# Performance work log

Measured on AMD Instinct MI355X. Metric: run time of the kernel, lower is better.

## Reference

```python
import jax, jax.numpy as jnp
import numpy as np
jax.config.update("jax_enable_x64", True)

PRIMES = [2654435761, 2246822519, 3266489917, 2028178513, 1220703125, 1610612741, 805306457, 402653189, 3674653429, 2860486313, 1073676287, 2971215073, 1500450271, 3267000013, 2654435789, 4049292737]
WINDOWS = [1, 2, 4, 8]
BUCKETS = 2000000
SIGN_BITS = 8
BOUNDARY = 2
OFFSETS = (1, 2, 3, 4, 5, 6, 7, 8)
CHUNK = 32


def layer_norm(x, w, b, eps=1e-5):
    m = jnp.mean(x, axis=-1, keepdims=True)
    v = jnp.var(x, axis=-1, keepdims=True)
    return (x - m) * jax.lax.rsqrt(v + eps) * w + b


def shift_right(tokens, off):
    T = tokens.shape[1]
    return jnp.pad(tokens, ((0, 0), (off, 0)))[:, :T]


def hash_scale(tokens, window):
    # rolling polynomial hash: XOR of prime-multiplied shifted tokens
    h = jnp.zeros_like(tokens)
    for i in range(window):
        off = i + 1
        if off >= tokens.shape[1]:
            continue
        h = h ^ (shift_right(tokens, off) * PRIMES[i % len(PRIMES)])
    return h % BUCKETS


def tiny_scan(x, gw, gb, iw, ib, ow, ob, lnw, lnb):
    # chunked cumsum-based linear recurrence h_t = a_t * h_{t-1} + (1-a_t) * u_t
    B, T, D = x.shape
    S = gw.shape[0]
    K = min(CHUNK, T)
    g = jax.nn.sigmoid(jnp.einsum('btd,sd->bts', x, gw) + gb)
    drive = (1.0 - g) * (jnp.einsum('btd,sd->bts', x, iw) + ib)
    nC = T // K  # T chosen divisible by CHUNK
    a = g.reshape(B, nC, K, S)
    b = drive.reshape(B, nC, K, S)
    log_a = jnp.log(jnp.maximum(a, 1e-6))
    cum_a = jnp.exp(jnp.cumsum(log_a, axis=2))             # [B,nC,K,S]
    inv_cum_a = 1.0 / jnp.maximum(cum_a, 1e-8)
    cum_wb = jnp.cumsum(b * inv_cum_a, axis=2)

    def step(h, cs):
        ca, cw = cs                                        # [B,K,S]
        out = ca * (h[:, None, :] + cw)
        return out[:, -1], out

    h0 = jnp.zeros((B, S), x.dtype)
    _, outs = jax.lax.scan(step, h0, (jnp.swapaxes(cum_a, 0, 1), jnp.swapaxes(cum_wb, 0, 1)))
    states = jnp.swapaxes(outs, 0, 1).reshape(B, T, S)
    y = jnp.einsum('bts,ds->btd', states, ow) + ob
    return layer_norm(x + y, lnw, lnb)


def forward(chars, byte_embed, table0, table1, table2, table3, cond_w, conv_w, conv_b,
            gate_w, gate_b, inpr_w, inpr_b, outpr_w, outpr_b, scan_ln_w, scan_ln_b,
            inp_w, inp_b, r_w1, r_w2, r_proj, r_ln_w, r_ln_b, out_w, out_b):
    tokens = chars.astype(jnp.int64)
    B, T = tokens.shape
    tables = [table0, table1, table2, table3]
    keys = [hash_scale(tokens, WINDOWS[s]) for s in range(4)]
    short = [tables[s][keys[s]] for s in range(BOUNDARY)]     # each [B,T,2]
    # condition long-scale keys on sign bits of short-scale features
    cond_logits = jnp.einsum('btd,sd->bts', jnp.concatenate(short, axis=-1), cond_w)
    bits = (cond_logits > 0).astype(jnp.int64)                # [B,T,8]
    cond_key = jnp.zeros((B, T), dtype=jnp.int64)
    for i in range(SIGN_BITS):
        cond_key = cond_key ^ (bits[..., i] * PRIMES[i])
    longe = [tables[s][(keys[s] ^ cond_key) % BUCKETS] for s in range(BOUNDARY, 4)]
    hash_feat = jnp.concatenate(short + longe, axis=-1)       # [B,T,8]
    # causal depthwise conv over hash features
    C = hash_feat.shape[-1]
    ht = jnp.swapaxes(hash_feat, 1, 2)                        # [B,C,T]
    Kc = conv_w.shape[-1]
    conv = jax.lax.conv_general_dilated(ht, conv_w, (1,), [(Kc - 1, 0)],
                                        dimension_numbers=('NCH', 'OIH', 'NCH'),
                                        feature_group_count=C)
    hash_feat = jax.nn.silu(jnp.swapaxes(conv + conv_b[None, :, None], 1, 2))
    byte_emb = byte_embed[tokens]                             # [B,T,64]
    # match features: equality with k-shifted sequence
    mfs = []
    for k in OFFSETS:
        m = (tokens == shift_right(tokens, k)).astype(jnp.float32)
        m = m.at[:, :k].set(0.0)
        mfs.append(m)
    mf = jnp.stack(mfs, axis=-1)                              # [B,T,8]
    h = jnp.concatenate([byte_emb, hash_feat, mf], axis=-1)   # [B,T,80]
    h = tiny_scan(h, gate_w, gate_b, inpr_w, inpr_b, outpr_w, outpr_b, scan_ln_w, scan_ln_b)
    h = jax.nn.silu(jnp.einsum('btd,hd->bth', h, inp_w) + inp_b)   # [B,T,256]
    hh = jnp.einsum('bth,dh->btd',
                    jax.nn.silu(jnp.einsum('btd,hd->bth', h, r_w1)) * jnp.einsum('btd,hd->bth', h, r_w2),
                    r_proj)
    h = layer_norm(hh + h, r_ln_w, r_ln_b)
    return jnp.einsum('bth,vh->btv', h, out_w) + out_b        # [B,T,1024]


def setup_inputs() -> dict:
    key = jax.random.key(0)
    ks = jax.random.split(key, 32)
    f32 = jnp.float32
    B, T, V, EB, S, D, H = 32, 2048, 1024, 64, 32, 80, 256

    def rn(k, shape, std):
        return jax.random.normal(k, shape, dtype=f32) * std

    return {
        'chars': jax.random.randint(ks[0], (B, T), 0, V, dtype=jnp.int64),
        'byte_embed': rn(ks[1], (V, EB), 0.02),
        'table0': rn(ks[2], (BUCKETS, 2), 0.02),
        'table1': rn(ks[3], (BUCKETS, 2), 0.02),
        'table2': rn(ks[4], (BUCKETS, 2), 0.02),
        'table3': rn(ks[5], (BUCKETS, 2), 0.02),
        'cond_w': rn(ks[6], (SIGN_BITS, 2 * BOUNDARY), 0.3),
        'conv_w': rn(ks[7], (8, 1, 8), 0.2),
        'conv_b': rn(ks[8], (8,), 0.02),
        'gate_w': rn(ks[9], (S, D), 0.1),
        'gate_b': rn(ks[10], (S,), 0.02),
        'inpr_w': rn(ks[11], (S, D), 0.1),
        'inpr_b': rn(ks[12], (S,), 0.02),
        'outpr_w': rn(ks[13], (D, S), 0.1),
        'outpr_b': rn(ks[14], (D,), 0.02),
        'scan_ln_w': jnp.ones((D,), f32),
        'scan_ln_b': jnp.zeros((D,), f32),
        'inp_w': rn(ks[15], (H, D), 0.1),
        'inp_b': rn(ks[16], (H,), 0.02),
        'r_w1': rn(ks[17], (H, H), 0.05),
        'r_w2': rn(ks[18], (H, H), 0.05),
        'r_proj': rn(ks[19], (H, H), 0.05),
        'r_ln_w': jnp.ones((H,), f32),
        'r_ln_b': jnp.zeros((H,), f32),
        'out_w': rn(ks[20], (V, H), 0.05),
        'out_b': rn(ks[21], (V,), 0.02),
    }


def reference(chars, byte_embed, table0, table1, table2, table3, cond_w, conv_w, conv_b,
              gate_w, gate_b, inpr_w, inpr_b, outpr_w, outpr_b, scan_ln_w, scan_ln_b,
              inp_w, inp_b, r_w1, r_w2, r_proj, r_ln_w, r_ln_b, out_w, out_b):
    return forward(chars, byte_embed, table0, table1, table2, table3, cond_w, conv_w, conv_b,
                   gate_w, gate_b, inpr_w, inpr_b, outpr_w, outpr_b, scan_ln_w, scan_ln_b,
                   inp_w, inp_b, r_w1, r_w2, r_proj, r_ln_w, r_ln_b, out_w, out_b)
```

## Files before the change

### kernel.cpp

```cpp
#include <hip/hip_runtime.h>

#define BB 32
#define TT 2048
#define SS 32
#define DD 80
#define HH 256
#define VV 1024
#define EBD 64

typedef unsigned short u16;
typedef __attribute__((ext_vector_type(8))) __bf16 bf16x8;
typedef __attribute__((ext_vector_type(4))) float f32x4;

#define MFMA(a, b, c) __builtin_amdgcn_mfma_f32_16x16x32_bf16(a, b, c, 0, 0, 0)

__device__ inline u16 f2bu(float f) {
    unsigned u = __float_as_uint(f);
    return (u16)((u + 0x7FFFu + ((u >> 16) & 1u)) >> 16);
}
__device__ inline __bf16 f2b(float f) {
    u16 r = f2bu(f);
    return __builtin_bit_cast(__bf16, r);
}
__device__ inline float b2f(u16 h) { return __uint_as_float(((unsigned)h) << 16); }

__device__ inline bf16x8 ldfrag(const u16* base, int row, int k0, int lane) {
    return *(const bf16x8*)(base + (size_t)row * 256 + k0 + ((lane >> 4) << 3));
}
__device__ inline bf16x8 ldfrag96(const u16* base, int row, int k0, int lane) {
    return *(const bf16x8*)(base + (size_t)row * 96 + k0 + ((lane >> 4) << 3));
}

__global__ __launch_bounds__(256) void k_prep(const float* __restrict__ w1,
                                              const float* __restrict__ w2,
                                              const float* __restrict__ wp,
                                              const float* __restrict__ ow,
                                              const float* __restrict__ iw,
                                              u16* __restrict__ wbf) {
    int i = blockIdx.x * 256 + threadIdx.x;
    if (i >= 483328) return;
    float v;
    if (i < 65536) v = w1[i];
    else if (i < 131072) v = w2[i - 65536];
    else if (i < 196608) v = wp[i - 131072];
    else if (i < 458752) v = ow[i - 196608];
    else {
        int j = i - 458752;
        int row = j / 96, col = j % 96;
        v = (col < 80) ? iw[row * 80 + col] : 0.f;
    }
    wbf[i] = f2bu(v);
}

__global__ __launch_bounds__(256) void k_hash(const int* __restrict__ tok,
                                              const float* __restrict__ t0,
                                              const float* __restrict__ t1,
                                              const float* __restrict__ t2,
                                              const float* __restrict__ t3,
                                              const float* __restrict__ cond_w,
                                              float* __restrict__ raw) {
    int idx = blockIdx.x * 256 + threadIdx.x;
    if (idx >= BB * TT) return;
    int b = idx / TT, t = idx % TT;
    const int* tr = tok + b * TT;

    unsigned long long tv[8];
#pragma unroll
    for (int i = 0; i < 8; i++) {
        int ts = t - 1 - i;
        tv[i] = (ts >= 0) ? (unsigned long long)(unsigned)tr[ts] : 0ull;
    }
    const unsigned long long P[8] = {2654435761ull, 2246822519ull, 3266489917ull,
                                     2028178513ull, 1220703125ull, 1610612741ull,
                                     805306457ull, 402653189ull};
    unsigned long long x = 0ull;
    x ^= tv[0] * P[0]; unsigned long long k0 = x % 2000000ull;
    x ^= tv[1] * P[1]; unsigned long long k1 = x % 2000000ull;
    x ^= tv[2] * P[2]; x ^= tv[3] * P[3]; unsigned long long k2 = x % 2000000ull;
    x ^= tv[4] * P[4]; x ^= tv[5] * P[5];
    x ^= tv[6] * P[6]; x ^= tv[7] * P[7]; unsigned long long k3 = x % 2000000ull;

    float f0 = t0[k0 * 2], f1 = t0[k0 * 2 + 1];
    float f2 = t1[k1 * 2], f3 = t1[k1 * 2 + 1];

    unsigned long long ck = 0ull;
#pragma unroll
    for (int j = 0; j < 8; j++) {
        float lg = f0 * cond_w[j * 4 + 0] + f1 * cond_w[j * 4 + 1] +
                   f2 * cond_w[j * 4 + 2] + f3 * cond_w[j * 4 + 3];
        if (lg > 0.f) ck ^= P[j];
    }
    unsigned long long lk2 = (k2 ^ ck) % 2000000ull;
    unsigned long long lk3 = (k3 ^ ck) % 2000000ull;

    float* o = raw + (size_t)idx * 8;
    o[0] = f0; o[1] = f1; o[2] = f2; o[3] = f3;
    o[4] = t2[lk2 * 2]; o[5] = t2[lk2 * 2 + 1];
    o[6] = t3[lk3 * 2]; o[7] = t3[lk3 * 2 + 1];
}

__global__ __launch_bounds__(256) void k_feat(const int* __restrict__ tok,
                                              const float* __restrict__ be,
                                              const float* __restrict__ raw,
                                              const float* __restrict__ conv_w,
                                              const float* __restrict__ conv_b,
                                              float* __restrict__ hf) {
    int idx = blockIdx.x * 256 + threadIdx.x;
    if (idx >= BB * TT) return;
    int b = idx / TT, t = idx % TT;
    const int* tr = tok + b * TT;
    float* o = hf + (size_t)idx * DD;

    int tk = tr[t];
    const float* ber = be + (size_t)tk * EBD;
#pragma unroll
    for (int q = 0; q < 16; q++) *(f32x4*)(o + q * 4) = *(const f32x4*)(ber + q * 4);

#pragma unroll
    for (int c = 0; c < 8; c++) {
        float acc = conv_b[c];
#pragma unroll
        for (int k = 0; k < 8; k++) {
            int ts = t - 7 + k;
            if (ts >= 0) acc += conv_w[c * 8 + k] * raw[((size_t)(b * TT + ts)) * 8 + c];
        }
        o[64 + c] = acc / (1.f + expf(-acc));
    }

#pragma unroll
    for (int k = 1; k <= 8; k++) {
        float m = (t >= k && tk == tr[t - k]) ? 1.f : 0.f;
        o[71 + k] = m;
    }
}

__global__ __launch_bounds__(256) void k_gates(const float* __restrict__ hf,
                                               const float* __restrict__ gw,
                                               const float* __restrict__ gb,
                                               const float* __restrict__ iw,
                                               const float* __restrict__ ib,
                                               float* __restrict__ Ag,
                                               float* __restrict__ Dr) {
    __shared__ float xs[64][DD];
    __shared__ float gws[32 * 81];
    __shared__ float iws[32 * 81];
    int blk = blockIdx.x;
    int b = blk >> 5;
    int t0 = (blk & 31) << 6;
    const float* src = hf + ((size_t)(b * TT + t0)) * DD;
    for (int i = threadIdx.x; i < 64 * DD; i += 256) xs[i / DD][i % DD] = src[i];
    for (int i = threadIdx.x; i < 32 * 80; i += 256) {
        int s = i / 80, d = i % 80;
        gws[s * 81 + d] = gw[i];
        iws[s * 81 + d] = iw[i];
    }
    __syncthreads();

    for (int p = threadIdx.x; p < 64 * SS; p += 256) {
        int s = p & 31, tt = p >> 5;
        float ga = gb[s], ia = ib[s];
        for (int d = 0; d < DD; d++) {
            float xv = xs[tt][d];
            ga += xv * gws[s * 81 + d];
            ia += xv * iws[s * 81 + d];
        }
        float g = 1.f / (1.f + expf(-ga));
        float drv = (1.f - g) * ia;
        size_t oo = ((size_t)(b * SS + s)) * TT + t0 + tt;
        Ag[oo] = g;
        Dr[oo] = drv;
    }
}

__global__ __launch_bounds__(64) void k_scan_par(const float* __restrict__ Ag,
                                                 const float* __restrict__ Dr,
                                                 float* __restrict__ st) {
    int bs = blockIdx.x;
    int b = bs >> 5, s = bs & 31;
    int c = threadIdx.x;
    const float* ar = Ag + (size_t)bs * TT + c * 32;
    const float* dr = Dr + (size_t)bs * TT + c * 32;

    float ca[32], cw[32];
    float lacc = 0.f, wacc = 0.f;
#pragma unroll
    for (int k = 0; k < 32; k += 4) {
        f32x4 av = *(const f32x4*)(ar + k);
        f32x4 dv = *(const f32x4*)(dr + k);
#pragma unroll
        for (int j = 0; j < 4; j++) {
            lacc += logf(fmaxf(av[j], 1e-6f));
            float cav = expf(lacc);
            ca[k + j] = cav;
            wacc += dv[j] / fmaxf(cav, 1e-8f);
            cw[k + j] = wacc;
        }
    }

    float A = ca[31];
    float Bc = ca[31] * wacc;
    for (int off = 1; off < 64; off <<= 1) {
        float Ap = __shfl_up(A, off, 64);
        float Bp = __shfl_up(Bc, off, 64);
        if (c >= off) {
            Bc = A * Bp + Bc;
            A = A * Ap;
        }
    }
    float h0 = __shfl_up(Bc, 1, 64);
    if (c == 0) h0 = 0.f;

    float* op = st + ((size_t)(b * TT + c * 32)) * SS + s;
#pragma unroll
    for (int k = 0; k < 32; k++)
        op[(size_t)k * SS] = ca[k] * (h0 + cw[k]);
}

__global__ __launch_bounds__(256) void k_post(const float* __restrict__ st,
                                              const float* __restrict__ hf,
                                              const float* __restrict__ ow,
                                              const float* __restrict__ ob,
                                              const float* __restrict__ lnw,
                                              const float* __restrict__ lnb,
                                              u16* __restrict__ h1p) {
    __shared__ float ows[DD * SS];
    for (int i = threadIdx.x; i < DD * SS; i += 256) ows[i] = ow[i];
    __syncthreads();

    int idx = blockIdx.x * 256 + threadIdx.x;
    if (idx >= BB * TT) return;
    const float* sp = st + (size_t)idx * SS;
    float sv[SS];
#pragma unroll
    for (int i = 0; i < SS; i += 4) {
        f32x4 v4 = *(const f32x4*)(sp + i);
        sv[i] = v4[0]; sv[i + 1] = v4[1]; sv[i + 2] = v4[2]; sv[i + 3] = v4[3];
    }
    const float* x = hf + (size_t)idx * DD;

    float s1 = 0.f, s2 = 0.f;
    for (int d = 0; d < DD; d++) {
        float acc = ob[d];
#pragma unroll
        for (int i = 0; i < SS; i++) acc += sv[i] * ows[d * SS + i];
        float v = acc + x[d];
        s1 += v; s2 += v * v;
    }
    float m = s1 * (1.f / DD);
    float var = s2 * (1.f / DD) - m * m;
    float rs = rsqrtf(var + 1e-5f);
    u16* o = h1p + (size_t)idx * 96;
    for (int d = 0; d < DD; d++) {
        float acc = ob[d];
#pragma unroll
        for (int i = 0; i < SS; i++) acc += sv[i] * ows[d * SS + i];
        float v = acc + x[d];
        o[d] = f2bu((v - m) * rs * lnw[d] + lnb[d]);
    }
    *(f32x4*)(o + 80) = f32x4{0.f, 0.f, 0.f, 0.f};
    *(f32x4*)(o + 88) = f32x4{0.f, 0.f, 0.f, 0.f};
}

#define SX 264
__global__ __launch_bounds__(256) void k_gmlp_f(const u16* __restrict__ h1p,
                                                const u16* __restrict__ iwb,
                                                const float* __restrict__ ibias,
                                                const u16* __restrict__ w1,
                                                const u16* __restrict__ w2,
                                                const u16* __restrict__ wp,
                                                const float* __restrict__ lnw,
                                                const float* __restrict__ lnb,
                                                u16* __restrict__ h3) {
    __shared__ u16 Xs[64 * SX];
    __shared__ u16 Us[64 * SX];
    __shared__ float redS[64][4], redQ[64][4];
    int lane = threadIdx.x & 63, wv = threadIdx.x >> 6;
    int r0 = blockIdx.x * 64;
    int g = lane >> 4, cl = lane & 15, rl = lane & 15;

    {
        int c0 = wv * 64;
        f32x4 acc[4][4] = {};
#pragma unroll
        for (int ks = 0; ks < 3; ks++) {
            int k0 = ks * 32;
            bf16x8 a[4];
#pragma unroll
            for (int mi = 0; mi < 4; mi++) a[mi] = ldfrag96(h1p, r0 + mi * 16 + rl, k0, lane);
#pragma unroll
            for (int ni = 0; ni < 4; ni++) {
                bf16x8 b = ldfrag96(iwb, c0 + ni * 16 + rl, k0, lane);
#pragma unroll
                for (int mi = 0; mi < 4; mi++) acc[mi][ni] = MFMA(a[mi], b, acc[mi][ni]);
            }
        }
#pragma unroll
        for (int ni = 0; ni < 4; ni++) {
            float bv = ibias[c0 + ni * 16 + cl];
#pragma unroll
            for (int mi = 0; mi < 4; mi++)
#pragma unroll
                for (int r = 0; r < 4; r++) {
                    float v = acc[mi][ni][r] + bv;
                    Xs[(mi * 16 + g * 4 + r) * SX + c0 + ni * 16 + cl] =
                        f2bu(v / (1.f + expf(-v)));
                }
        }
    }
    __syncthreads();

    for (int cg = 0; cg < 2; cg++) {
        int c0 = cg * 128 + wv * 32;
        f32x4 a1[4][2] = {}, a2[4][2] = {};
        for (int ks = 0; ks < 8; ks++) {
            int k0 = ks * 32 + (g << 3);
            bf16x8 a[4];
#pragma unroll
            for (int mi = 0; mi < 4; mi++)
                a[mi] = *(const bf16x8*)&Xs[(mi * 16 + rl) * SX + k0];
#pragma unroll
            for (int ni = 0; ni < 2; ni++) {
                bf16x8 b1 = ldfrag(w1, c0 + ni * 16 + rl, ks * 32, lane);
                bf16x8 b2 = ldfrag(w2, c0 + ni * 16 + rl, ks * 32, lane);
#pragma unroll
                for (int mi = 0; mi < 4; mi++) {
                    a1[mi][ni] = MFMA(a[mi], b1, a1[mi][ni]);
                    a2[mi][ni] = MFMA(a[mi], b2, a2[mi][ni]);
                }
            }
        }
#pragma unroll
        for (int mi = 0; mi < 4; mi++)
#pragma unroll
            for (int ni = 0; ni < 2; ni++)
#pragma unroll
                for (int r = 0; r < 4; r++) {
                    float v1 = a1[mi][ni][r], v2 = a2[mi][ni][r];
                    float u = v1 / (1.f + expf(-v1)) * v2;
                    Us[(mi * 16 + g * 4 + r) * SX + c0 + ni * 16 + cl] = f2bu(u);
                }
    }
    __syncthreads();

    {
        int c0 = wv * 64;
        f32x4 acc[4][4] = {};
        for (int ks = 0; ks < 8; ks++) {
            int k0 = ks * 32 + (g << 3);
            bf16x8 a[4];
#pragma unroll
            for (int mi = 0; mi < 4; mi++)
                a[mi] = *(const bf16x8*)&Us[(mi * 16 + rl) * SX + k0];
#pragma unroll
            for (int ni = 0; ni < 4; ni++) {
                bf16x8 b = ldfrag(wp, c0 + ni * 16 + rl, ks * 32, lane);
#pragma unroll
                for (int mi = 0; mi < 4; mi++) acc[mi][ni] = MFMA(a[mi], b, acc[mi][ni]);
            }
        }
#pragma unroll
        for (int mi = 0; mi < 4; mi++)
#pragma unroll
            for (int r = 0; r < 4; r++) {
                float s = 0.f, q = 0.f;
                int row = mi * 16 + g * 4 + r;
#pragma unroll
                for (int ni = 0; ni < 4; ni++) {
                    int col = c0 + ni * 16 + cl;
                    float v = acc[mi][ni][r] + b2f(Xs[row * SX + col]);
                    acc[mi][ni][r] = v;
                    s += v; q += v * v;
                }
                for (int m = 1; m < 16; m <<= 1) {
                    s += __shfl_xor(s, m, 64);
                    q += __shfl_xor(q, m, 64);
                }
                if (cl == 0) { redS[row][wv] = s; redQ[row][wv] = q; }
            }
        __syncthreads();

        float lw[4], lb[4];
#pragma unroll
        for (int ni = 0; ni < 4; ni++) {
            lw[ni] = lnw[c0 + ni * 16 + cl];
            lb[ni] = lnb[c0 + ni * 16 + cl];
        }
#pragma unroll
        for (int mi = 0; mi < 4; mi++)
#pragma unroll
            for (int r = 0; r < 4; r++) {
                int row = mi * 16 + g * 4 + r;
                float S = redS[row][0] + redS[row][1] + redS[row][2] + redS[row][3];
                float Q = redQ[row][0] + redQ[row][1] + redQ[row][2] + redQ[row][3];
                float m = S * (1.f / 256.f);
                float rs = rsqrtf(Q * (1.f / 256.f) - m * m + 1e-5f);
#pragma unroll
                for (int ni = 0; ni < 4; ni++) {
                    float y = (acc[mi][ni][r] - m) * rs * lw[ni] + lb[ni];
                    h3[(size_t)(r0 + row) * 256 + c0 + ni * 16 + cl] = f2bu(y);
                }
            }
    }
}

#define SA 40
__global__ __launch_bounds__(256) void k_out4(const u16* __restrict__ h3,
                                              const u16* __restrict__ ow,
                                              const float* __restrict__ bias,
                                              float* __restrict__ out) {
    __shared__ u16 As[2][128 * SA];
    __shared__ u16 Bs[2][128 * SA];
    int tid = threadIdx.x, lane = tid & 63, wv = tid >> 6;
    int r0 = blockIdx.x * 128;
    int wr = (wv >> 1) * 64, wc = (wv & 1) * 64;
    int rl = lane & 15, g = lane >> 4;

    int row0_ = tid >> 2, cc0_ = tid & 3;
    int row1_ = (tid + 256) >> 2, cc1_ = tid & 3;
    bf16x8 rA0, rA1, rB0, rB1;

#define LOADT(cg, kt)                                                                      \
    {                                                                                      \
        int kbase = (kt) * 32;                                                             \
        int c0g = (cg) * 128;                                                              \
        rA0 = *(const bf16x8*)(h3 + (size_t)(r0 + row0_) * 256 + kbase + cc0_ * 8);        \
        rA1 = *(const bf16x8*)(h3 + (size_t)(r0 + row1_) * 256 + kbase + cc1_ * 8);        \
        rB0 = *(const bf16x8*)(ow + (size_t)(c0g + row0_) * 256 + kbase + cc0_ * 8);       \
        rB1 = *(const bf16x8*)(ow + (size_t)(c0g + row1_) * 256 + kbase + cc1_ * 8);       \
    }
#define WRITET(buf)                                                                        \
    {                                                                                      \
        *(bf16x8*)&As[buf][row0_ * SA + cc0_ * 8] = rA0;                                   \
        *(bf16x8*)&As[buf][row1_ * SA + cc1_ * 8] = rA1;                                   \
        *(bf16x8*)&Bs[buf][row0_ * SA + cc0_ * 8] = rB0;                                   \
        *(bf16x8*)&Bs[buf][row1_ * SA + cc1_ * 8] = rB1;                                   \
    }

    for (int cg = 0; cg < 8; cg++) {
        LOADT(cg, 0);
        WRITET(0);
        f32x4 acc[4][4] = {};
        for (int kt = 0; kt < 8; kt++) {
            int buf = kt & 1;
            if (kt < 7) LOADT(cg, kt + 1);
            __syncthreads();
            bf16x8 a[4], b[4];
#pragma unroll
            for (int mi = 0; mi < 4; mi++)
                a[mi] = *(const bf16x8*)&As[buf][(wr + mi * 16 + rl) * SA + g * 8];
#pragma unroll
            for (int ni = 0; ni < 4; ni++)
                b[ni] = *(const bf16x8*)&Bs[buf][(wc + ni * 16 + rl) * SA + g * 8];
#pragma unroll
            for (int ni = 0; ni < 4; ni++)
#pragma unroll
                for (int mi = 0; mi < 4; mi++) acc[mi][ni] = MFMA(a[mi], b[ni], acc[mi][ni]);
            if (kt < 7) WRITET(buf ^ 1);
        }
        int c0g = cg * 128;
        int cl = lane & 15;
#pragma unroll
        for (int ni = 0; ni < 4; ni++) {
            float bv = bias[c0g + wc + ni * 16 + cl];
#pragma unroll
            for (int mi = 0; mi < 4; mi++)
#pragma unroll
                for (int r = 0; r < 4; r++)
                    out[(size_t)(r0 + wr + mi * 16 + g * 4 + r) * VV + c0g + wc + ni * 16 + cl] =
                        acc[mi][ni][r] + bv;
        }
        __syncthreads();
    }
#undef LOADT
#undef WRITET
}

extern "C" void kernel_launch(void* const* d_in, const int* in_sizes, int n_in,
                              void* d_out, int out_size, void* d_ws, size_t ws_size,
                              hipStream_t stream) {
    const int* chars        = (const int*)d_in[0];
    const float* byte_embed = (const float*)d_in[1];
    const float* table0     = (const float*)d_in[2];
    const float* table1     = (const float*)d_in[3];
    const float* table2     = (const float*)d_in[4];
    const float* table3     = (const float*)d_in[5];
    const float* cond_w     = (const float*)d_in[6];
    const float* conv_w     = (const float*)d_in[7];
    const float* conv_b     = (const float*)d_in[8];
    const float* gate_w     = (const float*)d_in[9];
    const float* gate_b     = (const float*)d_in[10];
    const float* inpr_w     = (const float*)d_in[11];
    const float* inpr_b     = (const float*)d_in[12];
    const float* outpr_w    = (const float*)d_in[13];
    const float* outpr_b    = (const float*)d_in[14];
    const float* scan_ln_w  = (const float*)d_in[15];
    const float* scan_ln_b  = (const float*)d_in[16];
    const float* inp_w      = (const float*)d_in[17];
    const float* inp_b      = (const float*)d_in[18];
    const float* r_w1       = (const float*)d_in[19];
    const float* r_w2       = (const float*)d_in[20];
    const float* r_proj     = (const float*)d_in[21];
    const float* r_ln_w     = (const float*)d_in[22];
    const float* r_ln_b     = (const float*)d_in[23];
    const float* out_w      = (const float*)d_in[24];
    const float* out_b      = (const float*)d_in[25];

    char* ws = (char*)d_ws;
    u16*   wbf = (u16*)(ws + 0);
    u16*   w1b = wbf;
    u16*   w2b = wbf + 65536;
    u16*   wpb = wbf + 131072;
    u16*   owb = wbf + 196608;
    u16*   iwb = wbf + 458752;
    float* hf  = (float*)(ws + 1048576);
    float* raw = (float*)(ws + 24117248);
    float* Ag  = (float*)(ws + 24117248);
    float* Dr  = (float*)(ws + 32505856);
    float* st  = (float*)(ws + 40894464);
    u16*   h1p = (u16*)(ws + 49283072);
    u16*   h3b = (u16*)(ws + 1048576);
    float* out = (float*)d_out;

    k_prep <<<1888, 256, 0, stream>>>(r_w1, r_w2, r_proj, out_w, inp_w, wbf);
    k_hash <<<256, 256, 0, stream>>>(chars, table0, table1, table2, table3, cond_w, raw);
    k_feat <<<256, 256, 0, stream>>>(chars, byte_embed, raw, conv_w, conv_b, hf);
    k_gates<<<1024, 256, 0, stream>>>(hf, gate_w, gate_b, inpr_w, inpr_b, Ag, Dr);
    k_scan_par<<<1024, 64, 0, stream>>>(Ag, Dr, st);
    k_post <<<256, 256, 0, stream>>>(st, hf, outpr_w, outpr_b, scan_ln_w, scan_ln_b, h1p);
    k_gmlp_f<<<1024, 256, 0, stream>>>(h1p, iwb, inp_b, w1b, w2b, wpb, r_ln_w, r_ln_b, h3b);
    k_out4 <<<512, 256, 0, stream>>>(h3b, owb, out_b, out);
}
```

Before: 339.7 us.

## Fuse feature build into gates kernel and output projection into gMLP kernel

Merges the feature-construction kernel into the gate/drive kernel, so embeddings, conv features and match flags go straight into shared memory while still being written to hf for the later residual. Also fuses the final vocabulary projection into the gMLP kernel: the layer-normed result stays in shared memory as bf16 and is multiplied by output weights read directly from global memory. This removes the h3 round trip through global memory and two kernel launches. The cost is heavier per-block work and uncached global B-fragment loads for the output GEMM, in place of the old double-buffered LDS tiling.

```diff
diff --git a/kernel.cpp b/kernel.cpp
--- a/kernel.cpp
+++ b/kernel.cpp
@@ -99,64 +99,68 @@
     o[6] = t3[lk3 * 2]; o[7] = t3[lk3 * 2 + 1];
 }
 
-__global__ __launch_bounds__(256) void k_feat(const int* __restrict__ tok,
-                                              const float* __restrict__ be,
-                                              const float* __restrict__ raw,
-                                              const float* __restrict__ conv_w,
-                                              const float* __restrict__ conv_b,
-                                              float* __restrict__ hf) {
-    int idx = blockIdx.x * 256 + threadIdx.x;
-    if (idx >= BB * TT) return;
-    int b = idx / TT, t = idx % TT;
-    const int* tr = tok + b * TT;
-    float* o = hf + (size_t)idx * DD;
-
-    int tk = tr[t];
-    const float* ber = be + (size_t)tk * EBD;
-#pragma unroll
-    for (int q = 0; q < 16; q++) *(f32x4*)(o + q * 4) = *(const f32x4*)(ber + q * 4);
-
-#pragma unroll
-    for (int c = 0; c < 8; c++) {
-        float acc = conv_b[c];
-#pragma unroll
-        for (int k = 0; k < 8; k++) {
-            int ts = t - 7 + k;
-            if (ts >= 0) acc += conv_w[c * 8 + k] * raw[((size_t)(b * TT + ts)) * 8 + c];
-        }
-        o[64 + c] = acc / (1.f + expf(-acc));
-    }
-
-#pragma unroll
-    for (int k = 1; k <= 8; k++) {
-        float m = (t >= k && tk == tr[t - k]) ? 1.f : 0.f;
-        o[71 + k] = m;
-    }
-}
-
-__global__ __launch_bounds__(256) void k_gates(const float* __restrict__ hf,
-                                               const float* __restrict__ gw,
-                                               const float* __restrict__ gb,
-                                               const float* __restrict__ iw,
-                                               const float* __restrict__ ib,
-                                               float* __restrict__ Ag,
-                                               float* __restrict__ Dr) {
+__global__ __launch_bounds__(256) void k_featgates(const int* __restrict__ tok,
+                                                   const float* __restrict__ be,
+                                                   const float* __restrict__ raw,
+                                                   const float* __restrict__ conv_w,
+                                                   const float* __restrict__ conv_b,
+                                                   const float* __restrict__ gw,
+                                                   const float* __restrict__ gb,
+                                                   const float* __restrict__ iw,
+                                                   const float* __restrict__ ib,
+                                                   float* __restrict__ hf,
+                                                   float* __restrict__ Ag,
+                                                   float* __restrict__ Dr) {
     __shared__ float xs[64][DD];
     __shared__ float gws[32 * 81];
     __shared__ float iws[32 * 81];
     int blk = blockIdx.x;
     int b = blk >> 5;
     int t0 = (blk & 31) << 6;
-    const float* src = hf + ((size_t)(b * TT + t0)) * DD;
-    for (int i = threadIdx.x; i < 64 * DD; i += 256) xs[i / DD][i % DD] = src[i];
-    for (int i = threadIdx.x; i < 32 * 80; i += 256) {
+    int tid = threadIdx.x;
+    const int* tr = tok + b * TT;
+
+    for (int i = tid; i < 32 * 80; i += 256) {
         int s = i / 80, d = i % 80;
         gws[s * 81 + d] = gw[i];
         iws[s * 81 + d] = iw[i];
     }
+
+    for (int i = tid; i < 1024; i += 256) {
+        int row = i >> 4, q = i & 15;
+        int t = t0 + row;
+        int tk = tr[t];
+        f32x4 v = *(const f32x4*)(be + (size_t)tk * EBD + q * 4);
+        *(f32x4*)&xs[row][q * 4] = v;
+        *(f32x4*)(hf + ((size_t)(b * TT + t)) * DD + q * 4) = v;
+    }
+
+    if (tid < 64) {
+        int t = t0 + tid;
+        int tk = tr[t];
+        float* o = hf + ((size_t)(b * TT + t)) * DD;
+#pragma unroll
+        for (int c = 0; c < 8; c++) {
+            float acc = conv_b[c];
+#pragma unroll
+            for (int k = 0; k < 8; k++) {
+                int ts = t - 7 + k;
+                if (ts >= 0) acc += conv_w[c * 8 + k] * raw[((size_t)(b * TT + ts)) * 8 + c];
+            }
+            float sv = acc / (1.f + expf(-acc));
+            xs[tid][64 + c] = sv;
+            o[64 + c] = sv;
+        }
+#pragma unroll
+        for (int k = 1; k <= 8; k++) {
+            float m = (t >= k && tk == tr[t - k]) ? 1.f : 0.f;
+            xs[tid][71 + k] = m;
+            o[71 + k] = m;
+        }
+    }
     __syncthreads();
 
-    for (int p = threadIdx.x; p < 64 * SS; p += 256) {
+    for (int p = tid; p < 64 * SS; p += 256) {
         int s = p & 31, tt = p >> 5;
         float ga = gb[s], ia = ib[s];
         for (int d = 0; d < DD; d++) {
@@ -262,15 +266,17 @@
 }
 
 #define SX 264
-__global__ __launch_bounds__(256) void k_gmlp_f(const u16* __restrict__ h1p,
-                                                const u16* __restrict__ iwb,
-                                                const float* __restrict__ ibias,
-                                                const u16* __restrict__ w1,
-                                                const u16* __restrict__ w2,
-                                                const u16* __restrict__ wp,
-                                                const float* __restrict__ lnw,
-                                                const float* __restrict__ lnb,
-                                                u16* __restrict__ h3) {
+__global__ __launch_bounds__(256) void k_gmlp_out(const u16* __restrict__ h1p,
+                                                  const u16* __restrict__ iwb,
+                                                  const float* __restrict__ ibias,
+                                                  const u16* __restrict__ w1,
+                                                  const u16* __restrict__ w2,
+                                                  const u16* __restrict__ wp,
+                                                  const float* __restrict__ lnw,
+                                                  const float* __restrict__ lnb,
+                                                  const u16* __restrict__ ow,
+                                                  const float* __restrict__ obias,
+                                                  float* __restrict__ out) {
     __shared__ u16 Xs[64 * SX];
     __shared__ u16 Us[64 * SX];
     __shared__ float redS[64][4], redQ[64][4];
@@ -337,7 +343,7 @@
                 for (int r = 0; r < 4; r++) {
                     float v1 = a1[mi][ni][r], v2 = a2[mi][ni][r];
                     float u = v1 / (1.f + expf(-v1)) * v2;
-                    Us[(mi * 16 + g * 4 + r) * SX + c0 + ni * 16 + cl] = f2bu(u);
+                    Us[(mi * 16 + g * 4 + r) * SX + cg * 128 + wv * 32 + ni * 16 + cl] = f2bu(u);
                 }
     }
     __syncthreads();
@@ -397,82 +403,39 @@
 #pragma unroll
                 for (int ni = 0; ni < 4; ni++) {
                     float y = (acc[mi][ni][r] - m) * rs * lw[ni] + lb[ni];
-                    h3[(size_t)(r0 + row) * 256 + c0 + ni * 16 + cl] = f2bu(y);
-                }
-            }
-    }
-}
-
-#define SA 40
-__global__ __launch_bounds__(256) void k_out4(const u16* __restrict__ h3,
-                                              const u16* __restrict__ ow,
-                                              const float* __restrict__ bias,
-                                              float* __restrict__ out) {
-    __shared__ u16 As[2][128 * SA];
-    __shared__ u16 Bs[2][128 * SA];
-    int tid = threadIdx.x, lane = tid & 63, wv = tid >> 6;
-    int r0 = blockIdx.x * 128;
-    int wr = (wv >> 1) * 64, wc = (wv & 1) * 64;
-    int rl = lane & 15, g = lane >> 4;
-
-    int row0_ = tid >> 2, cc0_ = tid & 3;
-    int row1_ = (tid + 256) >> 2, cc1_ = tid & 3;
-    bf16x8 rA0, rA1, rB0, rB1;
-
-#define LOADT(cg, kt)                                                                      \
-    {                                                                                      \
-        int kbase = (kt) * 32;                                                             \
-        int c0g = (cg) * 128;                                                              \
-        rA0 = *(const bf16x8*)(h3 + (size_t)(r0 + row0_) * 256 + kbase + cc0_ * 8);        \
-        rA1 = *(const bf16x8*)(h3 + (size_t)(r0 + row1_) * 256 + kbase + cc1_ * 8);        \
-        rB0 = *(const bf16x8*)(ow + (size_t)(c0g + row0_) * 256 + kbase + cc0_ * 8);       \
-        rB1 = *(const bf16x8*)(ow + (size_t)(c0g + row1_) * 256 + kbase + cc1_ * 8);       \
-    }
-#define WRITET(buf)                                                                        \
-    {                                                                                      \
-        *(bf16x8*)&As[buf][row0_ * SA + cc0_ * 8] = rA0;                                   \
-        *(bf16x8*)&As[buf][row1_ * SA + cc1_ * 8] = rA1;                                   \
-        *(bf16x8*)&Bs[buf][row0_ * SA + cc0_ * 8] = rB0;                                   \
-        *(bf16x8*)&Bs[buf][row1_ * SA + cc1_ * 8] = rB1;                                   \
-    }
-
-    for (int cg = 0; cg < 8; cg++) {
-        LOADT(cg, 0);
-        WRITET(0);
+                    Xs[row * SX + c0 + ni * 16 + cl] = f2bu(y);
+                }
+            }
+    }
+    __syncthreads();
+
+    for (int cg = 0; cg < 4; cg++) {
+        int c0 = cg * 256 + wv * 64;
         f32x4 acc[4][4] = {};
-        for (int kt = 0; kt < 8; kt++) {
-            int buf = kt & 1;
-            if (kt < 7) LOADT(cg, kt + 1);
-            __syncthreads();
-            bf16x8 a[4], b[4];
+        for (int ks = 0; ks < 8; ks++) {
+            int k0 = ks * 32 + (g << 3);
+            bf16x8 a[4];
 #pragma unroll
             for (int mi = 0; mi < 4; mi++)
-                a[mi] = *(const bf16x8*)&As[buf][(wr + mi * 16 + rl) * SA + g * 8];
-#pragma unroll
-            for (int ni = 0; ni < 4; ni++)
-                b[ni] = *(const bf16x8*)&Bs[buf][(wc + ni * 16 + rl) * SA + g * 8];
-#pragma unroll
-            for (int ni = 0; ni < 4; ni++)
-#pragma unroll
-                for (int mi = 0; mi < 4; mi++) acc[mi][ni] = MFMA(a[mi], b[ni], acc[mi][ni]);
-            if (kt < 7) WRITET(buf ^ 1);
-        }
-        int c0g = cg * 128;
-        int cl = lane & 15;
+                a[mi] = *(const bf16x8*)&Xs[(mi * 16 + rl) * SX + k0];
+#pragma unroll
+            for (int ni = 0; ni < 4; ni++) {
+                bf16x8 b = ldfrag(ow, c0 + ni * 16 + rl, ks * 32, lane);
+#pragma unroll
+                for (int mi = 0; mi < 4; mi++) acc[mi][ni] = MFMA(a[mi], b, acc[mi][ni]);
+            }
+        }
 #pragma unroll
         for (int ni = 0; ni < 4; ni++) {
-            float bv = bias[c0g + wc + ni * 16 + cl];
+            float bv = obias[c0 + ni * 16 + cl];
 #pragma unroll
             for (int mi = 0; mi < 4; mi++)
 #pragma unroll
                 for (int r = 0; r < 4; r++)
-                    out[(size_t)(r0 + wr + mi * 16 + g * 4 + r) * VV + c0g + wc + ni * 16 + cl] =
+                    out[(size_t)(r0 + mi * 16 + g * 4 + r) * VV + c0 + ni * 16 + cl] =
                         acc[mi][ni][r] + bv;
         }
-        __syncthreads();
-    }
-#undef LOADT
-#undef WRITET
+    }
 }
 
 extern "C" void kernel_launch(void* const* d_in, const int* in_sizes, int n_in,
@@ -513,20 +476,19 @@
     u16*   owb = wbf + 196608;
     u16*   iwb = wbf + 458752;
     float* hf  = (float*)(ws + 1048576);
-    float* raw = (float*)(ws + 24117248);
-    float* Ag  = (float*)(ws + 24117248);
-    float* Dr  = (float*)(ws + 32505856);
-    float* st  = (float*)(ws + 40894464);
-    u16*   h1p = (u16*)(ws + 49283072);
-    u16*   h3b = (u16*)(ws + 1048576);
+    float* raw = (float*)(ws + 23068672);
+    float* Ag  = (float*)(ws + 25165824);
+    float* Dr  = (float*)(ws + 33554432);
+    float* st  = (float*)(ws + 41943040);
+    u16*   h1p = (u16*)(ws + 50331648);
     float* out = (float*)d_out;
 
     k_prep <<<1888, 256, 0, stream>>>(r_w1, r_w2, r_proj, out_w, inp_w, wbf);
     k_hash <<<256, 256, 0, stream>>>(chars, table0, table1, table2, table3, cond_w, raw);
-    k_feat <<<256, 256, 0, stream>>>(chars, byte_embed, raw, conv_w, conv_b, hf);
-    k_gates<<<1024, 256, 0, stream>>>(hf, gate_w, gate_b, inpr_w, inpr_b, Ag, Dr);
+    k_featgates<<<1024, 256, 0, stream>>>(chars, byte_embed, raw, conv_w, conv_b,
+                                          gate_w, gate_b, inpr_w, inpr_b, hf, Ag, Dr);
     k_scan_par<<<1024, 64, 0, stream>>>(Ag, Dr, st);
     k_post <<<256, 256, 0, stream>>>(st, hf, outpr_w, outpr_b, scan_ln_w, scan_ln_b, h1p);
-    k_gmlp_f<<<1024, 256, 0, stream>>>(h1p, iwb, inp_b, w1b, w2b, wpb, r_ln_w, r_ln_b, h3b);
-    k_out4 <<<512, 256, 0, stream>>>(h3b, owb, out_b, out);
-}
+    k_gmlp_out<<<1024, 256, 0, stream>>>(h1p, iwb, inp_b, w1b, w2b, wpb,
+                                         r_ln_w, r_ln_b, owb, out_b, out);
+}
```

New measurement: 358.7 us. +5.6%, slower.
